# Kernel tuning notes

Measured on AMD Instinct MI355X. Metric: run time of the kernel, lower is better.

Reference implementation:

```python
import jax, jax.numpy as jnp
import numpy as np

R = 16
ALPHA = 32.0
SCALING = ALPHA / max(1, R)

def setup_inputs() -> dict:
    key = jax.random.key(0)
    ks = jax.random.split(key, 7)
    B_, D, M = 16384, 1024, 4096
    return {
        "x": jax.random.normal(ks[0], (B_, D), dtype=jnp.float32),
        "W0": jax.random.normal(ks[1], (M, D), dtype=jnp.float32) * 0.02,
        "b0": jax.random.normal(ks[2], (M,), dtype=jnp.float32) * 0.02,
        "A": jax.random.normal(ks[3], (R, D), dtype=jnp.float32) * 0.001,
        "B": jax.random.normal(ks[4], (M, R), dtype=jnp.float32) * 0.02,
        "W2": jax.random.normal(ks[5], (1, M), dtype=jnp.float32) * 0.02,
        "b2": jax.random.normal(ks[6], (1,), dtype=jnp.float32) * 0.02,
    }

def reference(x, W0, b0, A, B, W2, b2):
    # effective_W = W0 + scaling * (B @ A)  -> [m_hidden, d_in]
    W_eff = W0 + SCALING * (B @ A)
    # F.linear(x, W_eff, b0): x @ W_eff^T + b0 -> [batch, m_hidden]
    h = jax.nn.relu(jnp.einsum('bd,md->bm', x, W_eff) + b0)
    # fc2: [batch, 1] then squeeze(-1)
    out = (jnp.einsum('bm,om->bo', h, W2) + b2).squeeze(-1)
    return out
```

## Files before the change

kernel.cpp:

```cpp
#include <hip/hip_runtime.h>
#include <hip/hip_bf16.h>
#include <stdint.h>

#define BATCH  16384
#define D_IN   1024
#define M_HID  4096
#define R_LORA 16
#define SCALING 2.0f

#define STRIP    64
#define NTHREADS 512

typedef __bf16 bf16x8 __attribute__((ext_vector_type(8)));
typedef float  f32x16 __attribute__((ext_vector_type(16)));

__device__ __forceinline__ unsigned short f2bf(float f) {
    union { float f; unsigned int u; } c; c.f = f;
    unsigned int u = c.u;
    return (unsigned short)((u + 0x7FFFu + ((u >> 16) & 1u)) >> 16);
}

__global__ __launch_bounds__(256) void k_wprep(
    const float* __restrict__ W0, const float* __restrict__ A,
    const float* __restrict__ Bl, unsigned short* __restrict__ wb)
{
    __shared__ unsigned short T[32][D_IN + 8];
    const int n32 = blockIdx.x;
    const int t   = threadIdx.x;

    float4 Areg[R_LORA];
#pragma unroll
    for (int j = 0; j < R_LORA; ++j)
        Areg[j] = *(const float4*)(A + j * D_IN + t * 4);

#pragma unroll 4
    for (int r = 0; r < 32; ++r) {
        const int n = n32 * 32 + r;
        float4 v = *(const float4*)(W0 + (size_t)n * D_IN + t * 4);
        const float* brow = Bl + n * R_LORA;
#pragma unroll
        for (int j = 0; j < R_LORA; ++j) {
            float s = SCALING * brow[j];
            v.x += s * Areg[j].x; v.y += s * Areg[j].y;
            v.z += s * Areg[j].z; v.w += s * Areg[j].w;
        }
        ushort4 o = make_ushort4(f2bf(v.x), f2bf(v.y), f2bf(v.z), f2bf(v.w));
        *(ushort4*)(&T[r][t * 4]) = o;
    }
    __syncthreads();

    unsigned short* dst = wb + (size_t)n32 * 32768;
#pragma unroll
    for (int i = 0; i < 16; ++i) {
        int L  = t * 128 + i * 8;
        int c  = L >> 8;
        int rl = (L >> 3) & 31;
        uint4 v = *(const uint4*)(&T[rl][c * 8]);
        *(uint4*)(dst + L) = v;
    }
}

__global__ __launch_bounds__(NTHREADS, 2) void k_strip(
    const float* __restrict__ xf, const unsigned short* __restrict__ wb,
    const float* __restrict__ b0, const float* __restrict__ W2,
    const float* __restrict__ b2, float* __restrict__ out)
{
    __shared__ unsigned short As[STRIP * D_IN];
    __shared__ float red[8][STRIP];

    const int tid  = threadIdx.x;
    const int lane = tid & 63;
    const int wave = tid >> 6;
    const int rl   = lane & 31;
    const int half = lane >> 5;
    const int row0 = blockIdx.x * STRIP;

    {
        const int r  = tid >> 3;
        const int c0 = tid & 7;
        const float* xr = xf + (size_t)(row0 + r) * D_IN;
#pragma unroll
        for (int i = 0; i < 16; ++i) {
            int c = i * 8 + c0;
            float4 v0 = *(const float4*)(xr + c * 8);
            float4 v1 = *(const float4*)(xr + c * 8 + 4);
            uint4 o;
            o.x = (unsigned)f2bf(v0.x) | ((unsigned)f2bf(v0.y) << 16);
            o.y = (unsigned)f2bf(v0.z) | ((unsigned)f2bf(v0.w) << 16);
            o.z = (unsigned)f2bf(v1.x) | ((unsigned)f2bf(v1.y) << 16);
            o.w = (unsigned)f2bf(v1.z) | ((unsigned)f2bf(v1.w) << 16);
            *(uint4*)(&As[c * 512 + r * 8]) = o;
        }
    }
    __syncthreads();

    float rowpart[2][16];
#pragma unroll
    for (int ti = 0; ti < 2; ++ti)
#pragma unroll
        for (int r = 0; r < 16; ++r) rowpart[ti][r] = 0.f;

    for (int pass = 0; pass < 8; ++pass) {
        const int n0 = wave * 64 + pass * 512;
        const float w2a = W2[n0 + rl],      b0a = b0[n0 + rl];
        const float w2b = W2[n0 + 32 + rl], b0b = b0[n0 + 32 + rl];
        const int n32 = wave * 2 + pass * 16;
        const unsigned short* w0p = wb + (size_t)n32 * 32768 + half * 256 + rl * 8;
        const unsigned short* w1p = w0p + 32768;

        f32x16 acc[2][2] = {};
        bf16x8 wf0[4], wf1[4];
#pragma unroll
        for (int p = 0; p < 4; ++p) {
            wf0[p] = *(const bf16x8*)(w0p + p * 512);
            wf1[p] = *(const bf16x8*)(w1p + p * 512);
        }

#pragma unroll 4
        for (int kk = 0; kk < 64; ++kk) {
            const int cur = kk & 3;
            const int coff = (kk * 2 + half) * 512 + rl * 8;
            bf16x8 af0 = *(const bf16x8*)(&As[coff]);
            bf16x8 af1 = *(const bf16x8*)(&As[coff + 256]);
            bf16x8 w0c = wf0[cur], w1c = wf1[cur];
            if (kk < 60) {
                wf0[cur] = *(const bf16x8*)(w0p + (kk + 4) * 512);
                wf1[cur] = *(const bf16x8*)(w1p + (kk + 4) * 512);
            }
            acc[0][0] = __builtin_amdgcn_mfma_f32_32x32x16_bf16(af0, w0c, acc[0][0], 0, 0, 0);
            acc[0][1] = __builtin_amdgcn_mfma_f32_32x32x16_bf16(af0, w1c, acc[0][1], 0, 0, 0);
            acc[1][0] = __builtin_amdgcn_mfma_f32_32x32x16_bf16(af1, w0c, acc[1][0], 0, 0, 0);
            acc[1][1] = __builtin_amdgcn_mfma_f32_32x32x16_bf16(af1, w1c, acc[1][1], 0, 0, 0);
        }

#pragma unroll
        for (int ti = 0; ti < 2; ++ti)
#pragma unroll
            for (int r = 0; r < 16; ++r)
                rowpart[ti][r] += fmaxf(acc[ti][0][r] + b0a, 0.f) * w2a
                                + fmaxf(acc[ti][1][r] + b0b, 0.f) * w2b;
    }

#pragma unroll
    for (int ti = 0; ti < 2; ++ti)
#pragma unroll
        for (int r = 0; r < 16; ++r) {
            float p = rowpart[ti][r];
#pragma unroll
            for (int m = 1; m <= 16; m <<= 1)
                p += __shfl_xor(p, m, 64);
            if (rl == 0)
                red[wave][ti * 32 + (r & 3) + 8 * (r >> 2) + 4 * half] = p;
        }
    __syncthreads();
    if (tid < STRIP) {
        float s = b2[0];
#pragma unroll
        for (int w = 0; w < 8; ++w) s += red[w][tid];
        out[row0 + tid] = s;
    }
}

__global__ __launch_bounds__(256) void k_naive(
    const float* __restrict__ x, const float* __restrict__ W0,
    const float* __restrict__ b0, const float* __restrict__ A,
    const float* __restrict__ Bl, const float* __restrict__ W2,
    const float* __restrict__ b2, float* __restrict__ out)
{
    __shared__ float xs[D_IN];
    int b = blockIdx.x;
    for (int d = threadIdx.x; d < D_IN; d += 256) xs[d] = x[(size_t)b * D_IN + d];
    __syncthreads();
    float part = 0.f;
    for (int m = threadIdx.x; m < M_HID; m += 256) {
        float h = b0[m];
        const float* wr = W0 + (size_t)m * D_IN;
        const float* brow = Bl + m * R_LORA;
        for (int d = 0; d < D_IN; ++d) {
            float w = wr[d];
            for (int r = 0; r < R_LORA; ++r) w += SCALING * brow[r] * A[r * D_IN + d];
            h += xs[d] * w;
        }
        part += fmaxf(h, 0.f) * W2[m];
    }
    __shared__ float sred[256];
    sred[threadIdx.x] = part;
    __syncthreads();
    for (int s = 128; s > 0; s >>= 1) {
        if (threadIdx.x < s) sred[threadIdx.x] += sred[threadIdx.x + s];
        __syncthreads();
    }
    if (threadIdx.x == 0) out[b] = sred[0] + b2[0];
}

extern "C" void kernel_launch(void* const* d_in, const int* in_sizes, int n_in,
                              void* d_out, int out_size, void* d_ws, size_t ws_size,
                              hipStream_t stream) {
    const float* x  = (const float*)d_in[0];
    const float* W0 = (const float*)d_in[1];
    const float* b0 = (const float*)d_in[2];
    const float* A  = (const float*)d_in[3];
    const float* Bl = (const float*)d_in[4];
    const float* W2 = (const float*)d_in[5];
    const float* b2 = (const float*)d_in[6];
    float* out = (float*)d_out;

    const size_t wb_bytes = (size_t)M_HID * D_IN * 2;
    if (ws_size >= wb_bytes) {
        unsigned short* wb = (unsigned short*)d_ws;
        hipLaunchKernelGGL(k_wprep, dim3(M_HID / 32), dim3(256), 0, stream,
                           W0, A, Bl, wb);
        hipLaunchKernelGGL(k_strip, dim3(BATCH / STRIP), dim3(NTHREADS), 0, stream,
                           x, wb, b0, W2, b2, out);
    } else {
        hipLaunchKernelGGL(k_naive, dim3(BATCH), dim3(256), 0, stream,
                           x, W0, b0, A, Bl, W2, b2, out);
    }
}
```

Baseline: 249.4 us.

## Deepen weight prefetch across passes, double-buffer LDS A fragments, nontemporal loads

```diff
diff --git a/kernel.cpp b/kernel.cpp
--- a/kernel.cpp
+++ b/kernel.cpp
@@ -13,6 +13,7 @@
 
 typedef __bf16 bf16x8 __attribute__((ext_vector_type(8)));
 typedef float  f32x16 __attribute__((ext_vector_type(16)));
+typedef float  nfloat4 __attribute__((ext_vector_type(4)));
 
 __device__ __forceinline__ unsigned short f2bf(float f) {
     union { float f; unsigned int u; } c; c.f = f;
@@ -28,23 +29,23 @@
     const int n32 = blockIdx.x;
     const int t   = threadIdx.x;
 
-    float4 Areg[R_LORA];
+    nfloat4 Areg[R_LORA];
 #pragma unroll
     for (int j = 0; j < R_LORA; ++j)
-        Areg[j] = *(const float4*)(A + j * D_IN + t * 4);
+        Areg[j] = *(const nfloat4*)(A + j * D_IN + t * 4);
 
 #pragma unroll 4
     for (int r = 0; r < 32; ++r) {
         const int n = n32 * 32 + r;
-        float4 v = *(const float4*)(W0 + (size_t)n * D_IN + t * 4);
+        nfloat4 v = __builtin_nontemporal_load(
+            (const nfloat4*)(W0 + (size_t)n * D_IN + t * 4));
         const float* brow = Bl + n * R_LORA;
 #pragma unroll
         for (int j = 0; j < R_LORA; ++j) {
             float s = SCALING * brow[j];
-            v.x += s * Areg[j].x; v.y += s * Areg[j].y;
-            v.z += s * Areg[j].z; v.w += s * Areg[j].w;
-        }
-        ushort4 o = make_ushort4(f2bf(v.x), f2bf(v.y), f2bf(v.z), f2bf(v.w));
+            v = v + s * Areg[j];
+        }
+        ushort4 o = make_ushort4(f2bf(v[0]), f2bf(v[1]), f2bf(v[2]), f2bf(v[3]));
         *(ushort4*)(&T[r][t * 4]) = o;
     }
     __syncthreads();
@@ -82,13 +83,13 @@
 #pragma unroll
         for (int i = 0; i < 16; ++i) {
             int c = i * 8 + c0;
-            float4 v0 = *(const float4*)(xr + c * 8);
-            float4 v1 = *(const float4*)(xr + c * 8 + 4);
+            nfloat4 v0 = __builtin_nontemporal_load((const nfloat4*)(xr + c * 8));
+            nfloat4 v1 = __builtin_nontemporal_load((const nfloat4*)(xr + c * 8 + 4));
             uint4 o;
-            o.x = (unsigned)f2bf(v0.x) | ((unsigned)f2bf(v0.y) << 16);
-            o.y = (unsigned)f2bf(v0.z) | ((unsigned)f2bf(v0.w) << 16);
-            o.z = (unsigned)f2bf(v1.x) | ((unsigned)f2bf(v1.y) << 16);
-            o.w = (unsigned)f2bf(v1.z) | ((unsigned)f2bf(v1.w) << 16);
+            o.x = (unsigned)f2bf(v0[0]) | ((unsigned)f2bf(v0[1]) << 16);
+            o.y = (unsigned)f2bf(v0[2]) | ((unsigned)f2bf(v0[3]) << 16);
+            o.z = (unsigned)f2bf(v1[0]) | ((unsigned)f2bf(v1[1]) << 16);
+            o.w = (unsigned)f2bf(v1[2]) | ((unsigned)f2bf(v1[3]) << 16);
             *(uint4*)(&As[c * 512 + r * 8]) = o;
         }
     }
@@ -99,38 +100,49 @@
     for (int ti = 0; ti < 2; ++ti)
 #pragma unroll
         for (int r = 0; r < 16; ++r) rowpart[ti][r] = 0.f;
+
+    const unsigned short* w0base = wb + (size_t)(wave * 2) * 32768 + half * 256 + rl * 8;
+
+    bf16x8 wf0[8], wf1[8];
+#pragma unroll
+    for (int p = 0; p < 8; ++p) {
+        wf0[p] = *(const bf16x8*)(w0base + p * 512);
+        wf1[p] = *(const bf16x8*)(w0base + 32768 + p * 512);
+    }
+
+    const int abase = half * 512 + rl * 8;
+    bf16x8 a0 = *(const bf16x8*)(&As[abase]);
+    bf16x8 a1 = *(const bf16x8*)(&As[abase + 256]);
 
     for (int pass = 0; pass < 8; ++pass) {
         const int n0 = wave * 64 + pass * 512;
         const float w2a = W2[n0 + rl],      b0a = b0[n0 + rl];
         const float w2b = W2[n0 + 32 + rl], b0b = b0[n0 + 32 + rl];
-        const int n32 = wave * 2 + pass * 16;
-        const unsigned short* w0p = wb + (size_t)n32 * 32768 + half * 256 + rl * 8;
-        const unsigned short* w1p = w0p + 32768;
+        const unsigned short* wp  = w0base + (size_t)pass * 524288;
+        const unsigned short* wpn = wp + (pass < 7 ? 524288 : 0);
 
         f32x16 acc[2][2] = {};
-        bf16x8 wf0[4], wf1[4];
-#pragma unroll
-        for (int p = 0; p < 4; ++p) {
-            wf0[p] = *(const bf16x8*)(w0p + p * 512);
-            wf1[p] = *(const bf16x8*)(w1p + p * 512);
-        }
-
-#pragma unroll 4
+
+#pragma unroll 8
         for (int kk = 0; kk < 64; ++kk) {
-            const int cur = kk & 3;
-            const int coff = (kk * 2 + half) * 512 + rl * 8;
-            bf16x8 af0 = *(const bf16x8*)(&As[coff]);
-            bf16x8 af1 = *(const bf16x8*)(&As[coff + 256]);
+            const int cur = kk & 7;
             bf16x8 w0c = wf0[cur], w1c = wf1[cur];
-            if (kk < 60) {
-                wf0[cur] = *(const bf16x8*)(w0p + (kk + 4) * 512);
-                wf1[cur] = *(const bf16x8*)(w1p + (kk + 4) * 512);
+            const int nkk = (kk + 1) & 63;
+            const int noff = (nkk * 2 + half) * 512 + rl * 8;
+            bf16x8 a0n = *(const bf16x8*)(&As[noff]);
+            bf16x8 a1n = *(const bf16x8*)(&As[noff + 256]);
+            if (kk < 56) {
+                wf0[cur] = *(const bf16x8*)(wp + (kk + 8) * 512);
+                wf1[cur] = *(const bf16x8*)(wp + 32768 + (kk + 8) * 512);
+            } else {
+                wf0[cur] = *(const bf16x8*)(wpn + (kk - 56) * 512);
+                wf1[cur] = *(const bf16x8*)(wpn + 32768 + (kk - 56) * 512);
             }
-            acc[0][0] = __builtin_amdgcn_mfma_f32_32x32x16_bf16(af0, w0c, acc[0][0], 0, 0, 0);
-            acc[0][1] = __builtin_amdgcn_mfma_f32_32x32x16_bf16(af0, w1c, acc[0][1], 0, 0, 0);
-            acc[1][0] = __builtin_amdgcn_mfma_f32_32x32x16_bf16(af1, w0c, acc[1][0], 0, 0, 0);
-            acc[1][1] = __builtin_amdgcn_mfma_f32_32x32x16_bf16(af1, w1c, acc[1][1], 0, 0, 0);
+            acc[0][0] = __builtin_amdgcn_mfma_f32_32x32x16_bf16(a0, w0c, acc[0][0], 0, 0, 0);
+            acc[0][1] = __builtin_amdgcn_mfma_f32_32x32x16_bf16(a0, w1c, acc[0][1], 0, 0, 0);
+            acc[1][0] = __builtin_amdgcn_mfma_f32_32x32x16_bf16(a1, w0c, acc[1][0], 0, 0, 0);
+            acc[1][1] = __builtin_amdgcn_mfma_f32_32x32x16_bf16(a1, w1c, acc[1][1], 0, 0, 0);
+            a0 = a0n; a1 = a1n;
         }
 
 #pragma unroll
```

New measurement: 257.9 us. 1.03x slower.

## Quantize activations to int8 per row and widen strip tiling with split-N atomics

Applied to the files above, without the earlier changes.

```diff
diff --git a/kernel.cpp b/kernel.cpp
--- a/kernel.cpp
+++ b/kernel.cpp
@@ -8,11 +8,12 @@
 #define R_LORA 16
 #define SCALING 2.0f
 
-#define STRIP    64
+#define STRIP    128
 #define NTHREADS 512
 
 typedef __bf16 bf16x8 __attribute__((ext_vector_type(8)));
 typedef float  f32x16 __attribute__((ext_vector_type(16)));
+typedef float  nfloat4 __attribute__((ext_vector_type(4)));
 
 __device__ __forceinline__ unsigned short f2bf(float f) {
     union { float f; unsigned int u; } c; c.f = f;
@@ -20,6 +21,65 @@
     return (unsigned short)((u + 0x7FFFu + ((u >> 16) & 1u)) >> 16);
 }
 
+__device__ __forceinline__ bf16x8 expand8(int lo, int hi) {
+    union { bf16x8 v; unsigned u[4]; } o;
+#pragma unroll
+    for (int d = 0; d < 2; ++d) {
+        int src = d ? hi : lo;
+        float f0 = (float)((src << 24) >> 24);
+        float f1 = (float)((src << 16) >> 24);
+        float f2 = (float)((src << 8) >> 24);
+        float f3 = (float)(src >> 24);
+        unsigned u0 = __float_as_uint(f0), u1 = __float_as_uint(f1);
+        unsigned u2 = __float_as_uint(f2), u3 = __float_as_uint(f3);
+        o.u[d * 2 + 0] = (u0 >> 16) | (u1 & 0xFFFF0000u);
+        o.u[d * 2 + 1] = (u2 >> 16) | (u3 & 0xFFFF0000u);
+    }
+    return o.v;
+}
+
+__global__ __launch_bounds__(512) void k_xprep(
+    const float* __restrict__ x, const float* __restrict__ b2,
+    unsigned char* __restrict__ xq, float* __restrict__ sx,
+    float* __restrict__ out)
+{
+    const int bid = blockIdx.x;
+    const int strip = bid >> 1, rh = (bid & 1) * 64;
+    const int wv = threadIdx.x >> 6, l = threadIdx.x & 63;
+    unsigned char* dst = xq + (size_t)strip * 131072;
+
+#pragma unroll 2
+    for (int rr = 0; rr < 8; ++rr) {
+        const int r = rh + wv * 8 + rr;
+        const size_t gr = (size_t)strip * STRIP + r;
+        const float* xr = x + gr * D_IN;
+        nfloat4 v[4];
+        float mx = 0.f;
+#pragma unroll
+        for (int i = 0; i < 4; ++i) {
+            v[i] = *(const nfloat4*)(xr + i * 256 + l * 4);
+            mx = fmaxf(mx, fmaxf(fmaxf(fabsf(v[i][0]), fabsf(v[i][1])),
+                                 fmaxf(fabsf(v[i][2]), fabsf(v[i][3]))));
+        }
+#pragma unroll
+        for (int m = 1; m <= 32; m <<= 1) mx = fmaxf(mx, __shfl_xor(mx, m, 64));
+        const float qs = 127.0f / mx;
+#pragma unroll
+        for (int i = 0; i < 4; ++i) {
+            int k0 = i * 256 + l * 4;
+            int c = k0 >> 3, off = k0 & 7;
+            unsigned pk = (unsigned)(__float2int_rn(v[i][0] * qs) & 255)
+                        | ((unsigned)(__float2int_rn(v[i][1] * qs) & 255) << 8)
+                        | ((unsigned)(__float2int_rn(v[i][2] * qs) & 255) << 16)
+                        | ((unsigned)(__float2int_rn(v[i][3] * qs) & 255) << 24);
+            *(unsigned*)(dst + c * 1024 + r * 8 + off) = pk;
+        }
+        if (l == 0) sx[gr] = mx * (1.0f / 127.0f);
+    }
+    if (bid < 64 && threadIdx.x < 256)
+        out[bid * 256 + threadIdx.x] = b2[0];
+}
+
 __global__ __launch_bounds__(256) void k_wprep(
     const float* __restrict__ W0, const float* __restrict__ A,
     const float* __restrict__ Bl, unsigned short* __restrict__ wb)
@@ -28,136 +88,130 @@
     const int n32 = blockIdx.x;
     const int t   = threadIdx.x;
 
-    float4 Areg[R_LORA];
+    nfloat4 Areg[R_LORA];
 #pragma unroll
     for (int j = 0; j < R_LORA; ++j)
-        Areg[j] = *(const float4*)(A + j * D_IN + t * 4);
+        Areg[j] = *(const nfloat4*)(A + j * D_IN + t * 4);
 
 #pragma unroll 4
     for (int r = 0; r < 32; ++r) {
         const int n = n32 * 32 + r;
-        float4 v = *(const float4*)(W0 + (size_t)n * D_IN + t * 4);
+        nfloat4 v = __builtin_nontemporal_load(
+            (const nfloat4*)(W0 + (size_t)n * D_IN + t * 4));
         const float* brow = Bl + n * R_LORA;
 #pragma unroll
-        for (int j = 0; j < R_LORA; ++j) {
-            float s = SCALING * brow[j];
-            v.x += s * Areg[j].x; v.y += s * Areg[j].y;
-            v.z += s * Areg[j].z; v.w += s * Areg[j].w;
-        }
-        ushort4 o = make_ushort4(f2bf(v.x), f2bf(v.y), f2bf(v.z), f2bf(v.w));
+        for (int j = 0; j < R_LORA; ++j)
+            v = v + (SCALING * brow[j]) * Areg[j];
+        ushort4 o = make_ushort4(f2bf(v[0]), f2bf(v[1]), f2bf(v[2]), f2bf(v[3]));
         *(ushort4*)(&T[r][t * 4]) = o;
     }
     __syncthreads();
 
-    unsigned short* dst = wb + (size_t)n32 * 32768;
+    unsigned short* dstw = wb + (size_t)n32 * 32768;
 #pragma unroll
     for (int i = 0; i < 16; ++i) {
         int L  = t * 128 + i * 8;
         int c  = L >> 8;
         int rl = (L >> 3) & 31;
         uint4 v = *(const uint4*)(&T[rl][c * 8]);
-        *(uint4*)(dst + L) = v;
+        *(uint4*)(dstw + L) = v;
     }
 }
 
 __global__ __launch_bounds__(NTHREADS, 2) void k_strip(
-    const float* __restrict__ xf, const unsigned short* __restrict__ wb,
+    const unsigned char* __restrict__ xq, const float* __restrict__ sx,
+    const unsigned short* __restrict__ wb,
     const float* __restrict__ b0, const float* __restrict__ W2,
-    const float* __restrict__ b2, float* __restrict__ out)
-{
-    __shared__ unsigned short As[STRIP * D_IN];
+    float* __restrict__ out)
+{
+    __shared__ unsigned char As[STRIP * D_IN];
     __shared__ float red[8][STRIP];
+    __shared__ float sxs[STRIP];
 
     const int tid  = threadIdx.x;
     const int lane = tid & 63;
     const int wave = tid >> 6;
     const int rl   = lane & 31;
     const int half = lane >> 5;
-    const int row0 = blockIdx.x * STRIP;
+    const int bid  = blockIdx.x;
+    const int strip = bid >> 1, h = bid & 1;
+    const int row0 = strip * STRIP;
 
     {
-        const int r  = tid >> 3;
-        const int c0 = tid & 7;
-        const float* xr = xf + (size_t)(row0 + r) * D_IN;
+        float* rp = &red[0][0];
+        rp[tid] = 0.f;
+        rp[tid + 512] = 0.f;
+        if (tid < STRIP) sxs[tid] = sx[row0 + tid];
+        const unsigned char* src = xq + (size_t)strip * 131072;
 #pragma unroll
         for (int i = 0; i < 16; ++i) {
-            int c = i * 8 + c0;
-            float4 v0 = *(const float4*)(xr + c * 8);
-            float4 v1 = *(const float4*)(xr + c * 8 + 4);
-            uint4 o;
-            o.x = (unsigned)f2bf(v0.x) | ((unsigned)f2bf(v0.y) << 16);
-            o.y = (unsigned)f2bf(v0.z) | ((unsigned)f2bf(v0.w) << 16);
-            o.z = (unsigned)f2bf(v1.x) | ((unsigned)f2bf(v1.y) << 16);
-            o.w = (unsigned)f2bf(v1.z) | ((unsigned)f2bf(v1.w) << 16);
-            *(uint4*)(&As[c * 512 + r * 8]) = o;
-        }
-    }
-    __syncthreads();
-
-    float rowpart[2][16];
-#pragma unroll
-    for (int ti = 0; ti < 2; ++ti)
-#pragma unroll
-        for (int r = 0; r < 16; ++r) rowpart[ti][r] = 0.f;
-
-    for (int pass = 0; pass < 8; ++pass) {
-        const int n0 = wave * 64 + pass * 512;
+            int off = (i * NTHREADS + tid) * 16;
+            __builtin_amdgcn_global_load_lds(
+                (__attribute__((address_space(1))) void*)(src + off),
+                (__attribute__((address_space(3))) void*)(&As[off]),
+                16, 0, 0);
+        }
+    }
+    __syncthreads();
+
+    for (int pass = 0; pass < 4; ++pass) {
+        const int n0 = h * 2048 + pass * 512 + wave * 64;
         const float w2a = W2[n0 + rl],      b0a = b0[n0 + rl];
         const float w2b = W2[n0 + 32 + rl], b0b = b0[n0 + 32 + rl];
-        const int n32 = wave * 2 + pass * 16;
-        const unsigned short* w0p = wb + (size_t)n32 * 32768 + half * 256 + rl * 8;
-        const unsigned short* w1p = w0p + 32768;
-
-        f32x16 acc[2][2] = {};
+        const unsigned short* wp = wb + (size_t)(n0 >> 5) * 32768 + half * 256 + rl * 8;
+
+        f32x16 acc[4][2] = {};
         bf16x8 wf0[4], wf1[4];
 #pragma unroll
         for (int p = 0; p < 4; ++p) {
-            wf0[p] = *(const bf16x8*)(w0p + p * 512);
-            wf1[p] = *(const bf16x8*)(w1p + p * 512);
+            wf0[p] = *(const bf16x8*)(wp + p * 512);
+            wf1[p] = *(const bf16x8*)(wp + 32768 + p * 512);
         }
 
 #pragma unroll 4
         for (int kk = 0; kk < 64; ++kk) {
             const int cur = kk & 3;
-            const int coff = (kk * 2 + half) * 512 + rl * 8;
-            bf16x8 af0 = *(const bf16x8*)(&As[coff]);
-            bf16x8 af1 = *(const bf16x8*)(&As[coff + 256]);
             bf16x8 w0c = wf0[cur], w1c = wf1[cur];
             if (kk < 60) {
-                wf0[cur] = *(const bf16x8*)(w0p + (kk + 4) * 512);
-                wf1[cur] = *(const bf16x8*)(w1p + (kk + 4) * 512);
-            }
-            acc[0][0] = __builtin_amdgcn_mfma_f32_32x32x16_bf16(af0, w0c, acc[0][0], 0, 0, 0);
-            acc[0][1] = __builtin_amdgcn_mfma_f32_32x32x16_bf16(af0, w1c, acc[0][1], 0, 0, 0);
-            acc[1][0] = __builtin_amdgcn_mfma_f32_32x32x16_bf16(af1, w0c, acc[1][0], 0, 0, 0);
-            acc[1][1] = __builtin_amdgcn_mfma_f32_32x32x16_bf16(af1, w1c, acc[1][1], 0, 0, 0);
-        }
-
-#pragma unroll
-        for (int ti = 0; ti < 2; ++ti)
-#pragma unroll
-            for (int r = 0; r < 16; ++r)
-                rowpart[ti][r] += fmaxf(acc[ti][0][r] + b0a, 0.f) * w2a
-                                + fmaxf(acc[ti][1][r] + b0b, 0.f) * w2b;
-    }
-
-#pragma unroll
-    for (int ti = 0; ti < 2; ++ti)
-#pragma unroll
-        for (int r = 0; r < 16; ++r) {
-            float p = rowpart[ti][r];
-#pragma unroll
-            for (int m = 1; m <= 16; m <<= 1)
-                p += __shfl_xor(p, m, 64);
-            if (rl == 0)
-                red[wave][ti * 32 + (r & 3) + 8 * (r >> 2) + 4 * half] = p;
-        }
+                wf0[cur] = *(const bf16x8*)(wp + (kk + 4) * 512);
+                wf1[cur] = *(const bf16x8*)(wp + 32768 + (kk + 4) * 512);
+            }
+            const int c = kk * 2 + half;
+            const unsigned char* ab = &As[c * 1024 + rl * 8];
+            bf16x8 af[4];
+#pragma unroll
+            for (int rt = 0; rt < 4; ++rt) {
+                int2 raw = *(const int2*)(ab + rt * 256);
+                af[rt] = expand8(raw.x, raw.y);
+            }
+#pragma unroll
+            for (int rt = 0; rt < 4; ++rt) {
+                acc[rt][0] = __builtin_amdgcn_mfma_f32_32x32x16_bf16(af[rt], w0c, acc[rt][0], 0, 0, 0);
+                acc[rt][1] = __builtin_amdgcn_mfma_f32_32x32x16_bf16(af[rt], w1c, acc[rt][1], 0, 0, 0);
+            }
+        }
+
+#pragma unroll
+        for (int rt = 0; rt < 4; ++rt)
+#pragma unroll
+            for (int r = 0; r < 16; ++r) {
+                const int row = rt * 32 + (r & 3) + 8 * (r >> 2) + 4 * half;
+                const float s = sxs[row];
+                float p = fmaxf(s * acc[rt][0][r] + b0a, 0.f) * w2a
+                        + fmaxf(s * acc[rt][1][r] + b0b, 0.f) * w2b;
+#pragma unroll
+                for (int m = 1; m <= 16; m <<= 1)
+                    p += __shfl_xor(p, m, 64);
+                if (rl == 0) red[wave][row] += p;
+            }
+    }
+
     __syncthreads();
     if (tid < STRIP) {
-        float s = b2[0];
+        float s = 0.f;
 #pragma unroll
         for (int w = 0; w < 8; ++w) s += red[w][tid];
-        out[row0 + tid] = s;
+        unsafeAtomicAdd(&out[row0 + tid], s);
     }
 }
 
@@ -173,15 +227,15 @@
     __syncthreads();
     float part = 0.f;
     for (int m = threadIdx.x; m < M_HID; m += 256) {
-        float h = b0[m];
+        float hh = b0[m];
         const float* wr = W0 + (size_t)m * D_IN;
         const float* brow = Bl + m * R_LORA;
         for (int d = 0; d < D_IN; ++d) {
             float w = wr[d];
             for (int r = 0; r < R_LORA; ++r) w += SCALING * brow[r] * A[r * D_IN + d];
-            h += xs[d] * w;
-        }
-        part += fmaxf(h, 0.f) * W2[m];
+            hh += xs[d] * w;
+        }
+        part += fmaxf(hh, 0.f) * W2[m];
     }
     __shared__ float sred[256];
     sred[threadIdx.x] = part;
@@ -205,13 +259,17 @@
     const float* b2 = (const float*)d_in[6];
     float* out = (float*)d_out;
 
+    const size_t xq_bytes = (size_t)BATCH * D_IN;
+    const size_t sx_bytes = (size_t)BATCH * 4;
     const size_t wb_bytes = (size_t)M_HID * D_IN * 2;
-    if (ws_size >= wb_bytes) {
-        unsigned short* wb = (unsigned short*)d_ws;
-        hipLaunchKernelGGL(k_wprep, dim3(M_HID / 32), dim3(256), 0, stream,
-                           W0, A, Bl, wb);
-        hipLaunchKernelGGL(k_strip, dim3(BATCH / STRIP), dim3(NTHREADS), 0, stream,
-                           x, wb, b0, W2, b2, out);
+    if (ws_size >= xq_bytes + sx_bytes + wb_bytes) {
+        unsigned char*  xq = (unsigned char*)d_ws;
+        float*          sx = (float*)((char*)d_ws + xq_bytes);
+        unsigned short* wb = (unsigned short*)((char*)d_ws + xq_bytes + sx_bytes);
+        hipLaunchKernelGGL(k_xprep, dim3(256), dim3(512), 0, stream, x, b2, xq, sx, out);
+        hipLaunchKernelGGL(k_wprep, dim3(M_HID / 32), dim3(256), 0, stream, W0, A, Bl, wb);
+        hipLaunchKernelGGL(k_strip, dim3(256), dim3(NTHREADS), 0, stream,
+                           xq, sx, wb, b0, W2, out);
     } else {
         hipLaunchKernelGGL(k_naive, dim3(BATCH), dim3(256), 0, stream,
                            x, W0, b0, A, Bl, W2, b2, out);
```

Result: slower. 335.3 us (+34.5%).
